# Optimization experiments

Hardware: AMD Instinct MI355X
Metric: run time of the kernel (lower is better)

The kernel has to match this reference:

```python
import jax, jax.numpy as jnp
import numpy as np

N = 50000
E = 800000
NODE_DIM = 15
HID = 64
HEADS = 4
NEG_SLOPE = 0.2


def _add_self_loops(edge_index, n):
    loops = jnp.arange(n, dtype=edge_index.dtype)
    src = jnp.concatenate([edge_index[0], loops])
    dst = jnp.concatenate([edge_index[1], loops])
    return src, dst


def gat_conv(x, edge_index, W, att_src, att_dst, bias, concat):
    # x: [N, F_in]; W: [F_in, heads*out]; att_*: [heads, out]; bias: [heads*out] or [out]
    n = x.shape[0]
    heads, out_dim = att_src.shape
    src, dst = _add_self_loops(edge_index, n)
    h = (x @ W).reshape(n, heads, out_dim)              # [N, H, D]
    a_src = jnp.sum(h * att_src[None], axis=-1)          # [N, H]
    a_dst = jnp.sum(h * att_dst[None], axis=-1)          # [N, H]
    e = a_src[src] + a_dst[dst]                          # [E', H]
    e = jnp.where(e > 0, e, NEG_SLOPE * e)               # LeakyReLU(0.2)
    # segment softmax over incoming edges of each dst node
    m = jax.ops.segment_max(e, dst, num_segments=n)      # [N, H]
    m = jnp.where(jnp.isfinite(m), m, 0.0)
    w = jnp.exp(e - m[dst])                              # [E', H]
    z = jax.ops.segment_sum(w, dst, num_segments=n)      # [N, H]
    alpha = w / z[dst]                                   # [E', H]
    msg = alpha[:, :, None] * h[src]                     # [E', H, D]
    out = jax.ops.segment_sum(msg, dst, num_segments=n)  # [N, H, D]
    if concat:
        return out.reshape(n, heads * out_dim) + bias
    return out.mean(axis=1) + bias


def setup_inputs() -> dict:
    key = jax.random.key(0)
    ks = jax.random.split(key, 11)
    x = jax.random.normal(ks[0], (N, NODE_DIM), dtype=jnp.float32)
    edge_index = jax.random.randint(ks[1], (2, E), 0, N, dtype=jnp.int64)
    s1 = 1.0 / np.sqrt(NODE_DIM)
    s2 = 1.0 / np.sqrt(HEADS * HID)
    return {
        "x": x,
        "edge_index": edge_index,
        "W1": jax.random.normal(ks[2], (NODE_DIM, HEADS * HID), dtype=jnp.float32) * s1,
        "att_src1": jax.random.normal(ks[3], (HEADS, HID), dtype=jnp.float32) * s2,
        "att_dst1": jax.random.normal(ks[4], (HEADS, HID), dtype=jnp.float32) * s2,
        "b1": jnp.zeros((HEADS * HID,), dtype=jnp.float32),
        "W2": jax.random.normal(ks[5], (HEADS * HID, HID), dtype=jnp.float32) * s2,
        "att_src2": jax.random.normal(ks[6], (1, HID), dtype=jnp.float32) * s2,
        "att_dst2": jax.random.normal(ks[7], (1, HID), dtype=jnp.float32) * s2,
        "b2": jnp.zeros((HID,), dtype=jnp.float32),
    }


def reference(x, edge_index, W1, att_src1, att_dst1, b1, W2, att_src2, att_dst2, b2):
    h = gat_conv(x, edge_index, W1, att_src1, att_dst1, b1, concat=True)   # [N, 256]
    h = jax.nn.elu(h)
    # dropout p=0.2 skipped (eval mode)
    h = gat_conv(h, edge_index, W2, att_src2, att_dst2, b2, concat=True)   # heads=1 -> [N, 64]
    return h.mean(axis=0)                                                   # [64]
```

## Files before the change

### kernel.cpp

```cpp
#include <hip/hip_runtime.h>
#include <hip/hip_fp16.h>

#define NNODES 50000
#define NEDGES 800000
#define NEG_SLOPE 0.2f
#define NTOT (NEDGES + NNODES)
#define NB_NODE ((NNODES + 255) / 256)
#define CHUNK 4096
#define NCHUNK ((NEDGES + CHUNK - 1) / CHUNK)
#define CAPB 4800
#define CNTSTRIDE 16

typedef _Float16 half8 __attribute__((ext_vector_type(8)));
typedef _Float16 half4 __attribute__((ext_vector_type(4)));
typedef float f32x4 __attribute__((ext_vector_type(4)));

__global__ void setup_scatter(const float* __restrict__ x, const float* __restrict__ W1,
                              const float* __restrict__ att_src, const float* __restrict__ att_dst,
                              const float* __restrict__ W2,
                              const int* __restrict__ srcs, const int* __restrict__ dsts,
                              int* __restrict__ bucket_cnt, int* __restrict__ bucketbuf,
                              float* __restrict__ x16, float* __restrict__ asrc4,
                              float* __restrict__ adst4, _Float16* __restrict__ W2T) {
    int t = threadIdx.x;
    __shared__ unsigned short meta[CHUNK];
    __shared__ int lcnt[NB_NODE], lbase[NB_NODE];
    __shared__ float swa[16][4], swd[16][4];
    if (blockIdx.x < NCHUNK) {
        int b = blockIdx.x;
        for (int i = t; i < NB_NODE; i += 256) lcnt[i] = 0;
        __syncthreads();
        int e0 = b * CHUNK;
        int e1 = e0 + CHUNK; if (e1 > NEDGES) e1 = NEDGES;
        for (int e = e0 + t; e < e1; e += 256) {
            int d = dsts[e];
            meta[e - e0] = (unsigned short)d;
            atomicAdd(&lcnt[d >> 8], 1);
        }
        __syncthreads();
        for (int i = t; i < NB_NODE; i += 256) {
            int c = lcnt[i];
            lbase[i] = c ? atomicAdd(&bucket_cnt[i * CNTSTRIDE], c) : 0;
        }
        __syncthreads();
        for (int i = t; i < NB_NODE; i += 256) lcnt[i] = 0;
        __syncthreads();
        for (int e = e0 + t; e < e1; e += 256) {
            int dv = meta[e - e0];
            int bk = dv >> 8;
            int pos = lbase[bk] + atomicAdd(&lcnt[bk], 1);
            if (pos < CAPB) bucketbuf[bk * CAPB + pos] = ((dv & 255) << 16) | srcs[e];
        }
    } else {
        int b = blockIdx.x - NCHUNK;
        if (t < 128) {
            int k = (t & 63) >> 2, h = t & 3;
            float s = 0.f;
            if (k < 15) {
                const float* att = (t < 64) ? att_src : att_dst;
#pragma unroll 16
                for (int d = 0; d < 64; ++d)
                    s += W1[k * 256 + h * 64 + d] * att[h * 64 + d];
            }
            if (t < 64) swa[k][h] = s; else swd[k][h] = s;
        }
        int tid = b * 256 + t;
        if (tid < 64 * 256) {
            int n = tid >> 8, k = tid & 255;
            W2T[n * 256 + k] = (_Float16)W2[k * 64 + n];
        }
        __syncthreads();
        int nid = tid;
        if (nid < NNODES) {
            float xv[16];
#pragma unroll
            for (int k = 0; k < 15; ++k) xv[k] = x[nid * 15 + k];
            xv[15] = 0.f;
#pragma unroll
            for (int k = 0; k < 16; k += 4)
                *(float4*)(x16 + (size_t)nid * 16 + k) =
                    make_float4(xv[k], xv[k+1], xv[k+2], xv[k+3]);
            float ps[4] = {0.f, 0.f, 0.f, 0.f}, pd[4] = {0.f, 0.f, 0.f, 0.f};
#pragma unroll
            for (int k = 0; k < 15; ++k)
#pragma unroll
                for (int h = 0; h < 4; ++h) {
                    ps[h] += xv[k] * swa[k][h];
                    pd[h] += xv[k] * swd[k][h];
                }
            *(float4*)(asrc4 + nid * 4) = make_float4(ps[0], ps[1], ps[2], ps[3]);
            *(float4*)(adst4 + nid * 4) = make_float4(pd[0], pd[1], pd[2], pd[3]);
        }
    }
}

__global__ void scanA(const int* __restrict__ bucket_cnt, const int* __restrict__ bucketbuf,
                      int* __restrict__ rowstart, int* __restrict__ partials) {
    int b = blockIdx.x, t = threadIdx.x, lane = t & 63, wid = t >> 6;
    __shared__ int hist[256];
    __shared__ int ws[4];
    int i = b * 256 + t;
    hist[t] = (i < NNODES) ? 1 : 0;
    __syncthreads();
    int n = bucket_cnt[b * CNTSTRIDE]; if (n > CAPB) n = CAPB;
    const int* buf = bucketbuf + (size_t)b * CAPB;
    for (int j = t; j < n; j += 256)
        atomicAdd(&hist[buf[j] >> 16], 1);
    __syncthreads();
    int v = (i < NNODES) ? hist[t] : 0;
    int incl = v;
#pragma unroll
    for (int off = 1; off < 64; off <<= 1) {
        int u = __shfl_up(incl, off, 64);
        if (lane >= off) incl += u;
    }
    if (lane == 63) ws[wid] = incl;
    __syncthreads();
    int w0 = ws[0], w1 = ws[1], w2 = ws[2], w3 = ws[3];
    int woff = (wid > 0 ? w0 : 0) + (wid > 1 ? w1 : 0) + (wid > 2 ? w2 : 0);
    if (i < NNODES) rowstart[i] = woff + (incl - v);
    if (t == 0) partials[b] = w0 + w1 + w2 + w3;
}

__global__ void scanB(const int* __restrict__ partials, int* __restrict__ blockoff,
                      int* __restrict__ rowstart, int nb) {
    int t = threadIdx.x, lane = t & 63, wid = t >> 6;
    int v = (t < nb) ? partials[t] : 0;
    int incl = v;
#pragma unroll
    for (int off = 1; off < 64; off <<= 1) {
        int u = __shfl_up(incl, off, 64);
        if (lane >= off) incl += u;
    }
    __shared__ int ws[4];
    if (lane == 63) ws[wid] = incl;
    __syncthreads();
    int w0 = ws[0], w1 = ws[1], w2 = ws[2], w3 = ws[3];
    int woff = (wid > 0 ? w0 : 0) + (wid > 1 ? w1 : 0) + (wid > 2 ? w2 : 0);
    if (t < nb) blockoff[t] = woff + (incl - v);
    if (t == 0) rowstart[NNODES] = w0 + w1 + w2 + w3;
}

__global__ void local_sort(const int* __restrict__ bucket_cnt, const int* __restrict__ bucketbuf,
                           int* __restrict__ rowstart, const int* __restrict__ blockoff,
                           const int* __restrict__ partials,
                           const float4* __restrict__ asrc4, const float4* __restrict__ adst4,
                           int* __restrict__ srclist, float4* __restrict__ sw4) {
    int b = blockIdx.x, t = threadIdx.x;
    __shared__ int cur[256];
    __shared__ int local[8192];
    __shared__ float4 sadst[256];
    int boff = blockoff[b];
    int base = rowstart[b * 256] + boff;
    int idx = b * 256 + t;
    int fin = (idx < NNODES) ? rowstart[idx] + boff : 0;
    cur[t] = (idx < NNODES) ? (fin - base) : 0;
    int nid = idx;
    if (nid < NNODES) sadst[t] = adst4[nid];
    __syncthreads();
    if (nid < NNODES) rowstart[nid] = fin;
    if (nid < NNODES) {
        int pos = atomicAdd(&cur[t], 1);
        local[pos] = (t << 16) | nid;
    }
    int n = bucket_cnt[b * CNTSTRIDE]; if (n > CAPB) n = CAPB;
    const int* buf = bucketbuf + (size_t)b * CAPB;
    for (int i = t; i < n; i += 256) {
        int entry = buf[i];
        int pos = atomicAdd(&cur[entry >> 16], 1);
        local[pos] = entry;
    }
    __syncthreads();
    int total = partials[b];
    for (int i = t; i < total; i += 256) {
        int e = local[i];
        int s = e & 0xFFFF, dl = e >> 16;
        srclist[base + i] = s;
        float4 as = asrc4[s];
        float4 ad = sadst[dl];
        float e0 = as.x + ad.x, e1 = as.y + ad.y, e2 = as.z + ad.z, e3 = as.w + ad.w;
        e0 = fmaxf(e0, NEG_SLOPE * e0); e1 = fmaxf(e1, NEG_SLOPE * e1);
        e2 = fmaxf(e2, NEG_SLOPE * e2); e3 = fmaxf(e3, NEG_SLOPE * e3);
        sw4[base + i] = make_float4(__expf(e0), __expf(e1), __expf(e2), __expf(e3));
    }
}

__global__ void layer1_aggr(const float* __restrict__ x16, const int* __restrict__ rowstart,
                            const int* __restrict__ srclist, const float* __restrict__ sw4,
                            const float* __restrict__ W1, const float* __restrict__ b1,
                            __half* __restrict__ out1) {
    int wid = threadIdx.x >> 6, lane = threadIdx.x & 63;
    int nid = blockIdx.x * 4 + wid;
    int h = lane >> 4, k = lane & 15;
    int beg = __builtin_amdgcn_readfirstlane(rowstart[nid]);
    int end = __builtin_amdgcn_readfirstlane(rowstart[nid + 1]);
    int cnt = end - beg;
    float acc = 0.f, zs = 0.f;
    for (int c0 = 0; c0 < cnt; c0 += 64) {
        int rem = cnt - c0; if (rem > 64) rem = 64;
        int sv = (c0 + lane < cnt) ? srclist[beg + c0 + lane] : 0;
        int j = 0;
        for (; j + 8 <= rem; j += 8) {
#pragma unroll
            for (int u = 0; u < 8; ++u) {
                int s = __builtin_amdgcn_readlane(sv, j + u);
                float w = sw4[(size_t)(beg + c0 + j + u) * 4 + h];
                float xv = x16[s * 16 + k];
                zs += w;
                acc = fmaf(w, xv, acc);
            }
        }
        for (; j < rem; ++j) {
            int s = __builtin_amdgcn_readlane(sv, j);
            float w = sw4[(size_t)(beg + c0 + j) * 4 + h];
            zs += w;
            acc = fmaf(w, x16[s * 16 + k], acc);
        }
    }
    __shared__ float sacc[4][64];
    sacc[wid][lane] = acc * (1.f / zs);
    int c = lane, h2 = c >> 4;
    float o0 = 0.f, o1 = 0.f, o2 = 0.f, o3 = 0.f;
#pragma unroll
    for (int kk = 0; kk < 15; ++kk) {
        float a = sacc[wid][h2 * 16 + kk];
        float4 wv = *(const float4*)(W1 + kk * 256 + c * 4);
        o0 = fmaf(a, wv.x, o0); o1 = fmaf(a, wv.y, o1);
        o2 = fmaf(a, wv.z, o2); o3 = fmaf(a, wv.w, o3);
    }
    float4 bo = *(const float4*)(b1 + c * 4);
    o0 += bo.x; o1 += bo.y; o2 += bo.z; o3 += bo.w;
    o0 = o0 > 0.f ? o0 : __expf(o0) - 1.f;
    o1 = o1 > 0.f ? o1 : __expf(o1) - 1.f;
    o2 = o2 > 0.f ? o2 : __expf(o2) - 1.f;
    o3 = o3 > 0.f ? o3 : __expf(o3) - 1.f;
    half4 st;
    st[0] = (_Float16)o0; st[1] = (_Float16)o1; st[2] = (_Float16)o2; st[3] = (_Float16)o3;
    *(half4*)((_Float16*)out1 + (size_t)nid * 256 + c * 4) = st;
}


__global__ __launch_bounds__(256) void layer2_gemm(const __half* __restrict__ out1,
                                                   const _Float16* __restrict__ W2T,
                                                   __half* __restrict__ h2,
                                                   const float* __restrict__ att_src2,
                                                   const float* __restrict__ att_dst2,
                                                   float* __restrict__ as2,
                                                   float* __restrict__ ad2) {
    int w = threadIdx.x >> 6, lane = threadIdx.x & 63;
    int m16 = lane & 15, quad = lane >> 4;
    int r0 = blockIdx.x * 64 + w * 16;
    const _Float16* A = (const _Float16*)out1;
    f32x4 acc[4] = {{0.f,0.f,0.f,0.f},{0.f,0.f,0.f,0.f},{0.f,0.f,0.f,0.f},{0.f,0.f,0.f,0.f}};
    int row = r0 + m16; if (row >= NNODES) row = NNODES - 1;
#pragma unroll
    for (int k0 = 0; k0 < 256; k0 += 32) {
        half8 a = *(const half8*)(A + (size_t)row * 256 + k0 + quad * 8);
#pragma unroll
        for (int nt = 0; nt < 4; ++nt) {
            half8 b = *(const half8*)(W2T + (size_t)(nt * 16 + m16) * 256 + k0 + quad * 8);
            acc[nt] = __builtin_amdgcn_mfma_f32_16x16x32_f16(a, b, acc[nt], 0, 0, 0);
        }
    }
    __shared__ _Float16 tile[64][72];
#pragma unroll
    for (int nt = 0; nt < 4; ++nt)
#pragma unroll
        for (int r = 0; r < 4; ++r)
            tile[w * 16 + quad * 4 + r][nt * 16 + m16] = (_Float16)acc[nt][r];
    __syncthreads();
    int t = threadIdx.x;
    int trow = t >> 2, seg = t & 3;
    int rg = blockIdx.x * 64 + trow;
    if (rg < NNODES) {
        float4 v0 = *(float4*)&tile[trow][seg * 16];
        float4 v1 = *(float4*)&tile[trow][seg * 16 + 8];
        _Float16* dst = (_Float16*)h2 + (size_t)rg * 64 + seg * 16;
        *(float4*)dst = v0;
        *(float4*)(dst + 8) = v1;
        const _Float16* hv = &tile[trow][seg * 16];
        float ps = 0.f, pd = 0.f;
#pragma unroll
        for (int j = 0; j < 16; ++j) {
            float v = (float)hv[j];
            ps += v * att_src2[seg * 16 + j];
            pd += v * att_dst2[seg * 16 + j];
        }
        ps += __shfl_xor(ps, 1, 64); ps += __shfl_xor(ps, 2, 64);
        pd += __shfl_xor(pd, 1, 64); pd += __shfl_xor(pd, 2, 64);
        if (seg == 0) { as2[rg] = ps; ad2[rg] = pd; }
    }
}

__global__ void layer2_aggr(const __half* __restrict__ h2, const int* __restrict__ rowstart,
                            const int* __restrict__ srclist,
                            const float* __restrict__ as2, const float* __restrict__ ad2,
                            const float* __restrict__ b2, float* __restrict__ out2) {
    int wid = threadIdx.x >> 6, lane = threadIdx.x & 63;
    int nid = blockIdx.x * 4 + wid;
    int beg = __builtin_amdgcn_readfirstlane(rowstart[nid]);
    int end = __builtin_amdgcn_readfirstlane(rowstart[nid + 1]);
    int cnt = end - beg;
    float ad = ad2[nid];
    float acc = 0.f, zs = 0.f;
    for (int c0 = 0; c0 < cnt; c0 += 64) {
        int rem = cnt - c0; if (rem > 64) rem = 64;
        int sv = (c0 + lane < cnt) ? srclist[beg + c0 + lane] : 0;
        int j = 0;
        for (; j + 8 <= rem; j += 8) {
#pragma unroll
            for (int u = 0; u < 8; ++u) {
                int s = __builtin_amdgcn_readlane(sv, j + u);
                float e = as2[s] + ad;
                e = fmaxf(e, NEG_SLOPE * e);
                float w = __expf(e);
                float xv = __half2float(h2[(size_t)s * 64 + lane]);
                zs += w;
                acc = fmaf(w, xv, acc);
            }
        }
        for (; j < rem; ++j) {
            int s = __builtin_amdgcn_readlane(sv, j);
            float e = as2[s] + ad;
            e = fmaxf(e, NEG_SLOPE * e);
            float w = __expf(e);
            zs += w;
            acc = fmaf(w, __half2float(h2[(size_t)s * 64 + lane]), acc);
        }
    }
    out2[(size_t)nid * 64 + lane] = acc / zs + b2[lane];
}


__global__ void reduce_kernel(const float* __restrict__ out2, float* __restrict__ dout) {
    int t = threadIdx.x;
    int col = t & 63, sub = t >> 6;
    float acc = 0.f;
    for (int r = blockIdx.x * 4 + sub; r < NNODES; r += 256 * 4)
        acc += out2[r * 64 + col];
    __shared__ float sh[256];
    sh[t] = acc;
    __syncthreads();
    if (t < 64) {
        float v = sh[t] + sh[t + 64] + sh[t + 128] + sh[t + 192];
        atomicAdd(&dout[t], v * (1.0f / NNODES));
    }
}


extern "C" void kernel_launch(void* const* d_in, const int* in_sizes, int n_in,
                              void* d_out, int out_size, void* d_ws, size_t ws_size,
                              hipStream_t stream) {
    const float* x        = (const float*)d_in[0];
    const int*   ei       = (const int*)d_in[1];
    const float* W1       = (const float*)d_in[2];
    const float* att_src1 = (const float*)d_in[3];
    const float* att_dst1 = (const float*)d_in[4];
    const float* b1       = (const float*)d_in[5];
    const float* W2       = (const float*)d_in[6];
    const float* att_src2 = (const float*)d_in[7];
    const float* att_dst2 = (const float*)d_in[8];
    const float* b2       = (const float*)d_in[9];
    float* out = (float*)d_out;

    char* ws = (char*)d_ws;
    size_t off = 0;
    auto take = [&](size_t bytes) -> char* {
        char* p = ws + off;
        off = (off + bytes + 255) & ~(size_t)255;
        return p;
    };
    int*      bucket_cnt = (int*)take((size_t)NB_NODE * CNTSTRIDE * sizeof(int));
    int*      bucketbuf  = (int*)take((size_t)NB_NODE * CAPB * sizeof(int));
    int*      rowstart   = (int*)take((NNODES + 1) * sizeof(int));
    int*      partials   = (int*)take(256 * sizeof(int));
    int*      blockoff   = (int*)take(256 * sizeof(int));
    int*      srclist    = (int*)take(((size_t)NTOT + 64) * sizeof(int));
    float*    sw4        = (float*)take(((size_t)NTOT + 64) * 4 * sizeof(float));
    float*    x16        = (float*)take((size_t)NNODES * 16 * sizeof(float));
    float*    asrc4      = (float*)take((size_t)NNODES * 4 * sizeof(float));
    float*    adst4      = (float*)take((size_t)NNODES * 4 * sizeof(float));
    __half*   out1       = (__half*)take((size_t)NNODES * 256 * sizeof(__half));
    _Float16* W2T        = (_Float16*)take(64 * 256 * sizeof(_Float16));
    __half*   h2         = (__half*)take((size_t)NNODES * 64 * sizeof(__half));
    float*    as2        = (float*)take((size_t)NNODES * sizeof(float));
    float*    ad2        = (float*)take((size_t)NNODES * sizeof(float));
    float*    out2       = (float*)take((size_t)NNODES * 64 * sizeof(float));

    const int* srcs = ei;
    const int* dsts = ei + NEDGES;

    hipMemsetAsync(d_out, 0, 64 * sizeof(float), stream);
    hipMemsetAsync(bucket_cnt, 0, (size_t)NB_NODE * CNTSTRIDE * sizeof(int), stream);

    setup_scatter<<<NCHUNK + NB_NODE, 256, 0, stream>>>(x, W1, att_src1, att_dst1, W2,
                                                        srcs, dsts, bucket_cnt, bucketbuf,
                                                        x16, asrc4, adst4, W2T);
    scanA<<<NB_NODE, 256, 0, stream>>>(bucket_cnt, bucketbuf, rowstart, partials);
    scanB<<<1, 256, 0, stream>>>(partials, blockoff, rowstart, NB_NODE);
    local_sort<<<NB_NODE, 256, 0, stream>>>(bucket_cnt, bucketbuf, rowstart, blockoff, partials,
                                            (const float4*)asrc4, (const float4*)adst4,
                                            srclist, (float4*)sw4);

    layer1_aggr<<<NNODES / 4, 256, 0, stream>>>(x16, rowstart, srclist, sw4, W1, b1, out1);

    layer2_gemm<<<(NNODES + 63) / 64, 256, 0, stream>>>(out1, W2T, h2, att_src2, att_dst2,
                                                        as2, ad2);
    layer2_aggr<<<NNODES / 4, 256, 0, stream>>>(h2, rowstart, srclist, as2, ad2, b2, out2);

    reduce_kernel<<<256, 256, 0, stream>>>(out2, out);
}
```

Measured before the change: 234.2 us.

## Pack multiple nodes per wavefront in both GAT aggregation kernels

Layer-1 aggregation now handles four destination nodes per wavefront, one per 16-lane group. Each lane accumulates all four heads with float4 edge-weight loads, and a zero-padded sentinel weight slot covers out-of-range edges. Layer-2 aggregation handles two nodes per wavefront with half2 loads and accumulates in fp16 via hfma2. The aim is fewer idle lanes and wider memory accesses on low-degree nodes. The costs are divergence from looping to the group's maximum degree and reduced accumulation precision in layer 2.

```diff
diff --git a/kernel.cpp b/kernel.cpp
--- a/kernel.cpp
+++ b/kernel.cpp
@@ -10,6 +10,7 @@
 #define NCHUNK ((NEDGES + CHUNK - 1) / CHUNK)
 #define CAPB 4800
 #define CNTSTRIDE 16
+#define ZPAD (NTOT + 32)
 
 typedef _Float16 half8 __attribute__((ext_vector_type(8)));
 typedef _Float16 half4 __attribute__((ext_vector_type(4)));
@@ -150,6 +151,7 @@
     __shared__ int cur[256];
     __shared__ int local[8192];
     __shared__ float4 sadst[256];
+    if (b == 0 && t == 0) sw4[ZPAD] = make_float4(0.f, 0.f, 0.f, 0.f);
     int boff = blockoff[b];
     int base = rowstart[b * 256] + boff;
     int idx = b * 256 + t;
@@ -186,57 +188,90 @@
 }
 
 __global__ void layer1_aggr(const float* __restrict__ x16, const int* __restrict__ rowstart,
-                            const int* __restrict__ srclist, const float* __restrict__ sw4,
+                            const int* __restrict__ srclist, const float4* __restrict__ sw4,
                             const float* __restrict__ W1, const float* __restrict__ b1,
                             __half* __restrict__ out1) {
     int wid = threadIdx.x >> 6, lane = threadIdx.x & 63;
-    int nid = blockIdx.x * 4 + wid;
-    int h = lane >> 4, k = lane & 15;
-    int beg = __builtin_amdgcn_readfirstlane(rowstart[nid]);
-    int end = __builtin_amdgcn_readfirstlane(rowstart[nid + 1]);
-    int cnt = end - beg;
-    float acc = 0.f, zs = 0.f;
-    for (int c0 = 0; c0 < cnt; c0 += 64) {
-        int rem = cnt - c0; if (rem > 64) rem = 64;
-        int sv = (c0 + lane < cnt) ? srclist[beg + c0 + lane] : 0;
-        int j = 0;
-        for (; j + 8 <= rem; j += 8) {
-#pragma unroll
-            for (int u = 0; u < 8; ++u) {
-                int s = __builtin_amdgcn_readlane(sv, j + u);
-                float w = sw4[(size_t)(beg + c0 + j + u) * 4 + h];
-                float xv = x16[s * 16 + k];
-                zs += w;
-                acc = fmaf(w, xv, acc);
-            }
-        }
-        for (; j < rem; ++j) {
-            int s = __builtin_amdgcn_readlane(sv, j);
-            float w = sw4[(size_t)(beg + c0 + j) * 4 + h];
-            zs += w;
-            acc = fmaf(w, x16[s * 16 + k], acc);
-        }
-    }
-    __shared__ float sacc[4][64];
-    sacc[wid][lane] = acc * (1.f / zs);
+    int g = lane >> 4, k = lane & 15;
+    int base = blockIdx.x * 16 + wid * 4;
+    int nid = base + g;
+    int beg = rowstart[nid];
+    int cnt = rowstart[nid + 1] - beg;
+    int cmax = cnt;
+    cmax = max(cmax, __shfl_xor(cmax, 16, 64));
+    cmax = max(cmax, __shfl_xor(cmax, 32, 64));
+    cmax = __builtin_amdgcn_readfirstlane(cmax);
+    int gb = g * 16;
+    float4 acc = {0.f, 0.f, 0.f, 0.f};
+    float4 zs  = {0.f, 0.f, 0.f, 0.f};
+    for (int c0 = 0; c0 < cmax; c0 += 16) {
+        int sv = (c0 + k < cnt) ? srclist[beg + c0 + k] : 0;
+        int bmax = cmax - c0; if (bmax > 16) bmax = 16;
+        for (int j = 0; j < bmax; j += 4) {
+            int i0 = c0 + j;
+            int s0 = __shfl(sv, gb + j + 0, 64);
+            int s1 = __shfl(sv, gb + j + 1, 64);
+            int s2 = __shfl(sv, gb + j + 2, 64);
+            int s3 = __shfl(sv, gb + j + 3, 64);
+            int w0i = (i0 + 0 < cnt) ? beg + i0 + 0 : ZPAD;
+            int w1i = (i0 + 1 < cnt) ? beg + i0 + 1 : ZPAD;
+            int w2i = (i0 + 2 < cnt) ? beg + i0 + 2 : ZPAD;
+            int w3i = (i0 + 3 < cnt) ? beg + i0 + 3 : ZPAD;
+            float4 w0 = sw4[w0i];
+            float4 w1 = sw4[w1i];
+            float4 w2 = sw4[w2i];
+            float4 w3 = sw4[w3i];
+            float x0 = x16[s0 * 16 + k];
+            float x1 = x16[s1 * 16 + k];
+            float x2 = x16[s2 * 16 + k];
+            float x3 = x16[s3 * 16 + k];
+            zs.x += (w0.x + w1.x) + (w2.x + w3.x);
+            zs.y += (w0.y + w1.y) + (w2.y + w3.y);
+            zs.z += (w0.z + w1.z) + (w2.z + w3.z);
+            zs.w += (w0.w + w1.w) + (w2.w + w3.w);
+            acc.x = fmaf(w3.x, x3, fmaf(w2.x, x2, fmaf(w1.x, x1, fmaf(w0.x, x0, acc.x))));
+            acc.y = fmaf(w3.y, x3, fmaf(w2.y, x2, fmaf(w1.y, x1, fmaf(w0.y, x0, acc.y))));
+            acc.z = fmaf(w3.z, x3, fmaf(w2.z, x2, fmaf(w1.z, x1, fmaf(w0.z, x0, acc.z))));
+            acc.w = fmaf(w3.w, x3, fmaf(w2.w, x2, fmaf(w1.w, x1, fmaf(w0.w, x0, acc.w))));
+        }
+    }
+    __shared__ float sacc[4][4][64];
+    sacc[wid][g][0 * 16 + k] = acc.x / zs.x;
+    sacc[wid][g][1 * 16 + k] = acc.y / zs.y;
+    sacc[wid][g][2 * 16 + k] = acc.z / zs.z;
+    sacc[wid][g][3 * 16 + k] = acc.w / zs.w;
     int c = lane, h2 = c >> 4;
-    float o0 = 0.f, o1 = 0.f, o2 = 0.f, o3 = 0.f;
+    float4 bo = *(const float4*)(b1 + c * 4);
+    float4 o0 = bo, o1 = bo, o2 = bo, o3 = bo;
 #pragma unroll
     for (int kk = 0; kk < 15; ++kk) {
-        float a = sacc[wid][h2 * 16 + kk];
         float4 wv = *(const float4*)(W1 + kk * 256 + c * 4);
-        o0 = fmaf(a, wv.x, o0); o1 = fmaf(a, wv.y, o1);
-        o2 = fmaf(a, wv.z, o2); o3 = fmaf(a, wv.w, o3);
-    }
-    float4 bo = *(const float4*)(b1 + c * 4);
-    o0 += bo.x; o1 += bo.y; o2 += bo.z; o3 += bo.w;
-    o0 = o0 > 0.f ? o0 : __expf(o0) - 1.f;
-    o1 = o1 > 0.f ? o1 : __expf(o1) - 1.f;
-    o2 = o2 > 0.f ? o2 : __expf(o2) - 1.f;
-    o3 = o3 > 0.f ? o3 : __expf(o3) - 1.f;
-    half4 st;
-    st[0] = (_Float16)o0; st[1] = (_Float16)o1; st[2] = (_Float16)o2; st[3] = (_Float16)o3;
-    *(half4*)((_Float16*)out1 + (size_t)nid * 256 + c * 4) = st;
+        float a0 = sacc[wid][0][h2 * 16 + kk];
+        float a1 = sacc[wid][1][h2 * 16 + kk];
+        float a2 = sacc[wid][2][h2 * 16 + kk];
+        float a3 = sacc[wid][3][h2 * 16 + kk];
+        o0.x = fmaf(a0, wv.x, o0.x); o0.y = fmaf(a0, wv.y, o0.y);
+        o0.z = fmaf(a0, wv.z, o0.z); o0.w = fmaf(a0, wv.w, o0.w);
+        o1.x = fmaf(a1, wv.x, o1.x); o1.y = fmaf(a1, wv.y, o1.y);
+        o1.z = fmaf(a1, wv.z, o1.z); o1.w = fmaf(a1, wv.w, o1.w);
+        o2.x = fmaf(a2, wv.x, o2.x); o2.y = fmaf(a2, wv.y, o2.y);
+        o2.z = fmaf(a2, wv.z, o2.z); o2.w = fmaf(a2, wv.w, o2.w);
+        o3.x = fmaf(a3, wv.x, o3.x); o3.y = fmaf(a3, wv.y, o3.y);
+        o3.z = fmaf(a3, wv.z, o3.z); o3.w = fmaf(a3, wv.w, o3.w);
+    }
+    float4 ov[4] = {o0, o1, o2, o3};
+#pragma unroll
+    for (int gp = 0; gp < 4; ++gp) {
+        float p0 = ov[gp].x, p1 = ov[gp].y, p2 = ov[gp].z, p3 = ov[gp].w;
+        p0 = p0 > 0.f ? p0 : __expf(p0) - 1.f;
+        p1 = p1 > 0.f ? p1 : __expf(p1) - 1.f;
+        p2 = p2 > 0.f ? p2 : __expf(p2) - 1.f;
+        p3 = p3 > 0.f ? p3 : __expf(p3) - 1.f;
+        half4 st;
+        st[0] = (_Float16)p0; st[1] = (_Float16)p1;
+        st[2] = (_Float16)p2; st[3] = (_Float16)p3;
+        *(half4*)((_Float16*)out1 + (size_t)(base + gp) * 256 + c * 4) = st;
+    }
 }
 
 
@@ -297,38 +332,40 @@
                             const float* __restrict__ as2, const float* __restrict__ ad2,
                             const float* __restrict__ b2, float* __restrict__ out2) {
     int wid = threadIdx.x >> 6, lane = threadIdx.x & 63;
-    int nid = blockIdx.x * 4 + wid;
-    int beg = __builtin_amdgcn_readfirstlane(rowstart[nid]);
-    int end = __builtin_amdgcn_readfirstlane(rowstart[nid + 1]);
-    int cnt = end - beg;
+    int sub = lane >> 5, l2 = lane & 31;
+    int nid = blockIdx.x * 8 + wid * 2 + sub;
+    int beg = rowstart[nid];
+    int cnt = rowstart[nid + 1] - beg;
+    int cmax = max(cnt, __shfl_xor(cnt, 32, 64));
+    cmax = __builtin_amdgcn_readfirstlane(cmax);
     float ad = ad2[nid];
-    float acc = 0.f, zs = 0.f;
-    for (int c0 = 0; c0 < cnt; c0 += 64) {
-        int rem = cnt - c0; if (rem > 64) rem = 64;
-        int sv = (c0 + lane < cnt) ? srclist[beg + c0 + lane] : 0;
-        int j = 0;
-        for (; j + 8 <= rem; j += 8) {
-#pragma unroll
-            for (int u = 0; u < 8; ++u) {
-                int s = __builtin_amdgcn_readlane(sv, j + u);
+    const __half2* hp = (const __half2*)h2;
+    __half2 acc2 = __float2half2_rn(0.f);
+    float zs = 0.f;
+    int sb = sub * 32;
+    for (int c0 = 0; c0 < cmax; c0 += 32) {
+        int sv = (c0 + l2 < cnt) ? srclist[beg + c0 + l2] : 0;
+        int bmax = cmax - c0; if (bmax > 32) bmax = 32;
+        for (int j = 0; j < bmax; j += 4) {
+#pragma unroll
+            for (int u = 0; u < 4; ++u) {
+                int jj = j + u;
+                int s = __shfl(sv, sb + jj, 64);
+                bool valid = (c0 + jj) < cnt;
                 float e = as2[s] + ad;
                 e = fmaxf(e, NEG_SLOPE * e);
-                float w = __expf(e);
-                float xv = __half2float(h2[(size_t)s * 64 + lane]);
-                zs += w;
-                acc = fmaf(w, xv, acc);
+                float wv = valid ? __expf(e) : 0.f;
+                __half2 gv = hp[s * 32 + l2];
+                zs += wv;
+                acc2 = __hfma2(__float2half2_rn(wv), gv, acc2);
             }
         }
-        for (; j < rem; ++j) {
-            int s = __builtin_amdgcn_readlane(sv, j);
-            float e = as2[s] + ad;
-            e = fmaxf(e, NEG_SLOPE * e);
-            float w = __expf(e);
-            zs += w;
-            acc = fmaf(w, __half2float(h2[(size_t)s * 64 + lane]), acc);
-        }
-    }
-    out2[(size_t)nid * 64 + lane] = acc / zs + b2[lane];
+    }
+    float2 f = __half22float2(acc2);
+    float rz = 1.f / zs;
+    float2 bo = *(const float2*)(b2 + l2 * 2);
+    *(float2*)(out2 + (size_t)nid * 64 + l2 * 2) = make_float2(f.x * rz + bo.x,
+                                                               f.y * rz + bo.y);
 }
 
 
@@ -402,11 +439,12 @@
                                             (const float4*)asrc4, (const float4*)adst4,
                                             srclist, (float4*)sw4);
 
-    layer1_aggr<<<NNODES / 4, 256, 0, stream>>>(x16, rowstart, srclist, sw4, W1, b1, out1);
+    layer1_aggr<<<NNODES / 16, 256, 0, stream>>>(x16, rowstart, srclist, (const float4*)sw4,
+                                                 W1, b1, out1);
 
     layer2_gemm<<<(NNODES + 63) / 64, 256, 0, stream>>>(out1, W2T, h2, att_src2, att_dst2,
                                                         as2, ad2);
-    layer2_aggr<<<NNODES / 4, 256, 0, stream>>>(h2, rowstart, srclist, as2, ad2, b2, out2);
+    layer2_aggr<<<NNODES / 8, 256, 0, stream>>>(h2, rowstart, srclist, as2, ad2, b2, out2);
 
     reduce_kernel<<<256, 256, 0, stream>>>(out2, out);
 }
```

After: 204.2 us. 12.8% less time.
